# Kernel optimization log

Hardware: AMD Instinct MI355X
Metric: run time of the kernel (lower is better)

Reference implementation:

```python
import jax, jax.numpy as jnp
import numpy as np

G = 8          # num_groups
GIN = 2048 // G   # group_in_features
GOUT = 2048 // G  # group_out_features


def setup_inputs() -> dict:
    key = jax.random.key(0)
    kx, kw, kb = jax.random.split(key, 3)
    x = jax.random.normal(kx, (8192, 2048), dtype=jnp.float32)
    # per-group linear params, torch nn.Linear default init scale ~ U(-1/sqrt(fan_in), ...)
    bound = 1.0 / np.sqrt(GIN)
    W = jax.random.uniform(kw, (G, GIN, GOUT), minval=-bound, maxval=bound, dtype=jnp.float32)
    b = jax.random.uniform(kb, (G, GOUT), minval=-bound, maxval=bound, dtype=jnp.float32)
    # rational activation coeffs, init p=[1,0,0,0], q=[1,0,0] per group
    p = jnp.tile(jnp.array([1.0, 0.0, 0.0, 0.0], dtype=jnp.float32), (G, 1))
    q = jnp.tile(jnp.array([1.0, 0.0, 0.0], dtype=jnp.float32), (G, 1))
    return {"x": x, "W": W, "b": b, "p": p, "q": q}


def _rational(y, p, q):
    # y: [N, G, GOUT]; p: [G, 4]; q: [G, 3] -> broadcast over N and GOUT
    p = p[None, :, :, None]  # [1,G,4,1]
    q = q[None, :, :, None]  # [1,G,3,1]
    y2 = y * y
    y3 = y2 * y
    num = p[:, :, 0] + p[:, :, 1] * y + p[:, :, 2] * y2 + p[:, :, 3] * y3
    den = 1.0 + jnp.abs(q[:, :, 0] * y + q[:, :, 1] * y2 + q[:, :, 2] * y3)
    return num / den


def reference(x, W, b, p, q):
    N = x.shape[0]
    xg = x.reshape(N, G, GIN)                       # chunk along last dim
    y = jnp.einsum('ngi,gio->ngo', xg, W) + b[None]  # grouped GEMM, [N,G,GOUT]
    out = _rational(y, p, q)
    return out.reshape(N, G * GOUT)                 # cat along last dim
```

## Files before the change

### kernel.cpp

```cpp
#include <hip/hip_runtime.h>
#include <hip/hip_bf16.h>

#define G_ 8
#define GIN_ 256
#define GOUT_ 256
#define NROWS_ 8192
#define LDX_ 2048

typedef __attribute__((ext_vector_type(4))) float f32x4;
typedef __attribute__((ext_vector_type(8))) short bf16x8;

__global__ __launch_bounds__(256) void wprep_kernel(const float* __restrict__ W,
                                                    __hip_bfloat16* __restrict__ Wt) {
    __shared__ float tile[64][65];
    const int bid = blockIdx.x;
    const int g  = bid >> 4;
    const int kt = (bid >> 2) & 3;
    const int ct = bid & 3;
    const float* Wg = W + g * (GIN_ * GOUT_);
    __hip_bfloat16* Wo = Wt + (size_t)g * (GIN_ * GOUT_);
    const int lane_o = threadIdx.x & 63;
    const int sub    = threadIdx.x >> 6;
#pragma unroll
    for (int r = 0; r < 16; ++r) {
        int i = r * 4 + sub;
        tile[i][lane_o] = Wg[(kt * 64 + i) * GOUT_ + ct * 64 + lane_o];
    }
    __syncthreads();
    const int col = threadIdx.x & 63;
    const int kgb = threadIdx.x >> 6;
#pragma unroll
    for (int h = 0; h < 2; ++h) {
        const int kg    = kgb + h * 4;
        const int kglob = kt * 64 + kg * 8;
        const int c     = kglob >> 5;
        const int quad  = (kglob >> 3) & 3;
        const int colg  = ct * 64 + col;
        const int cb    = colg >> 4;
        const int c16   = colg & 15;
        union { __hip_bfloat16 hh[8]; bf16x8 v; } cv;
#pragma unroll
        for (int j = 0; j < 8; ++j)
            cv.hh[j] = __float2bfloat16(tile[kg * 8 + j][col]);
        *(bf16x8*)(Wo + (size_t)(c * 16 + cb) * 512 + c16 * 32 + quad * 8) = cv.v;
    }
}

__device__ __forceinline__ bf16x8 cvt8(const f32x4 a, const f32x4 b) {
    union { __hip_bfloat16 h[8]; bf16x8 v; } u;
    u.h[0] = __float2bfloat16(a.x); u.h[1] = __float2bfloat16(a.y);
    u.h[2] = __float2bfloat16(a.z); u.h[3] = __float2bfloat16(a.w);
    u.h[4] = __float2bfloat16(b.x); u.h[5] = __float2bfloat16(b.y);
    u.h[6] = __float2bfloat16(b.z); u.h[7] = __float2bfloat16(b.w);
    return u.v;
}

__global__ __launch_bounds__(512, 4) void gkan_kernel(const float* __restrict__ x,
                                                      const __hip_bfloat16* __restrict__ Wt,
                                                      const float* __restrict__ bias,
                                                      const float* __restrict__ pc,
                                                      const float* __restrict__ qc,
                                                      float* __restrict__ out) {
    __shared__ __align__(16) float As[2][32 * 256];

    const int bid  = blockIdx.x;
    const int g    = bid & 7;
    const int row0 = (bid >> 3) * 128;

    const int t    = threadIdx.x;
    const int wave = t >> 6;
    const int lane = t & 63;
    const int lm   = lane & 15;
    const int q    = lane >> 4;

    const float* xbase = x + (size_t)row0 * LDX_ + g * GIN_;
    const int gsrc = (lane & ~7) | ((lane & 7) ^ wave);

#define DMA_SLAB(s, buf)                                                      \
    {                                                                         \
        const float* xs_ = xbase + (size_t)(s) * 32 * LDX_;                   \
        _Pragma("unroll")                                                     \
        for (int r_ = 0; r_ < 4; ++r_) {                                      \
            const float* src_ = xs_ + (size_t)(r_ * 8 + wave) * LDX_ + gsrc * 4; \
            __builtin_amdgcn_global_load_lds(                                 \
                (const __attribute__((address_space(1))) void*)src_,          \
                (__attribute__((address_space(3))) void*)                     \
                    ((char*)As + (buf) * 32768 + r_ * 8192 + t * 16),         \
                16, 0, 0);                                                    \
        }                                                                     \
    }

    DMA_SLAB(0, 0);

    const __hip_bfloat16* bp = Wt + (size_t)g * (GIN_ * GOUT_)
                                  + (wave * 2) * 512 + lm * 32 + q * 8;
    bf16x8 B0[8], B1[8];
#pragma unroll
    for (int c = 0; c < 8; ++c) {
        B0[c] = *(const bf16x8*)(bp + (size_t)c * (16 * 512));
        B1[c] = *(const bf16x8*)(bp + (size_t)c * (16 * 512) + 512);
    }

    f32x4 bb4[2];
    int col0[2];
#pragma unroll
    for (int nt = 0; nt < 2; ++nt) {
        col0[nt] = g * GOUT_ + wave * 32 + nt * 16 + q * 4;
        bb4[nt]  = *(const f32x4*)(bias + col0[nt]);
    }
    const float p0 = pc[g * 4 + 0], p1 = pc[g * 4 + 1];
    const float p2 = pc[g * 4 + 2], p3 = pc[g * 4 + 3];
    const float q0 = qc[g * 3 + 0], q1 = qc[g * 3 + 1], q2 = qc[g * 3 + 2];

    asm volatile("s_waitcnt vmcnt(0)\n\ts_barrier" ::: "memory");

#pragma unroll 1
    for (int s = 0; s < 4; ++s) {
        const int buf = s & 1;

        if (s < 3) DMA_SLAB(s + 1, buf ^ 1);

        f32x4 acc[2][2] = {};
        const char* ab = (const char*)As + buf * 32768;
#pragma unroll
        for (int c = 0; c < 8; ++c) {
            bf16x8 af[2];
#pragma unroll
            for (int mt = 0; mt < 2; ++mt) {
                const int rr  = mt * 16 + lm;
                const int gg0 = c * 8 + ((q * 2)     ^ (lm & 7));
                const int gg1 = c * 8 + ((q * 2 + 1) ^ (lm & 7));
                const f32x4 lo = *(const f32x4*)(ab + rr * 1024 + gg0 * 16);
                const f32x4 hi = *(const f32x4*)(ab + rr * 1024 + gg1 * 16);
                af[mt] = cvt8(lo, hi);
            }
            acc[0][0] = __builtin_amdgcn_mfma_f32_16x16x32_bf16(B0[c], af[0], acc[0][0], 0, 0, 0);
            acc[0][1] = __builtin_amdgcn_mfma_f32_16x16x32_bf16(B1[c], af[0], acc[0][1], 0, 0, 0);
            acc[1][0] = __builtin_amdgcn_mfma_f32_16x16x32_bf16(B0[c], af[1], acc[1][0], 0, 0, 0);
            acc[1][1] = __builtin_amdgcn_mfma_f32_16x16x32_bf16(B1[c], af[1], acc[1][1], 0, 0, 0);
        }

#pragma unroll
        for (int mt = 0; mt < 2; ++mt) {
            const int row_o = row0 + s * 32 + mt * 16 + lm;
#pragma unroll
            for (int nt = 0; nt < 2; ++nt) {
                f32x4 o;
#pragma unroll
                for (int r = 0; r < 4; ++r) {
                    const float y   = acc[mt][nt][r] + bb4[nt][r];
                    const float num = p0 + y * (p1 + y * (p2 + y * p3));
                    const float den = 1.0f + fabsf(y * (q0 + y * (q1 + y * q2)));
                    o[r] = num * __builtin_amdgcn_rcpf(den);
                }
                *(f32x4*)(out + (size_t)row_o * LDX_ + col0[nt]) = o;
            }
        }

        if (s < 3)
            asm volatile("s_waitcnt vmcnt(4)\n\ts_barrier" ::: "memory");
    }
#undef DMA_SLAB
}

extern "C" void kernel_launch(void* const* d_in, const int* in_sizes, int n_in,
                              void* d_out, int out_size, void* d_ws, size_t ws_size,
                              hipStream_t stream) {
    const float* x = (const float*)d_in[0];
    const float* W = (const float*)d_in[1];
    const float* b = (const float*)d_in[2];
    const float* p = (const float*)d_in[3];
    const float* q = (const float*)d_in[4];
    float* out = (float*)d_out;

    __hip_bfloat16* Wt = (__hip_bfloat16*)d_ws;

    wprep_kernel<<<128, 256, 0, stream>>>(W, Wt);
    gkan_kernel<<<512, 512, 0, stream>>>(x, Wt, b, p, q, out);
}
```

Baseline: 127.3 us.

## Deepen x prefetch pipeline to four 16-row LDS buffers with fully unrolled schedule

```diff
diff --git a/kernel.cpp b/kernel.cpp
--- a/kernel.cpp
+++ b/kernel.cpp
@@ -61,7 +61,7 @@
                                                       const float* __restrict__ pc,
                                                       const float* __restrict__ qc,
                                                       float* __restrict__ out) {
-    __shared__ __align__(16) float As[2][32 * 256];
+    __shared__ __align__(16) float As[4][16 * 256];
 
     const int bid  = blockIdx.x;
     const int g    = bid & 7;
@@ -76,21 +76,52 @@
     const float* xbase = x + (size_t)row0 * LDX_ + g * GIN_;
     const int gsrc = (lane & ~7) | ((lane & 7) ^ wave);
 
-#define DMA_SLAB(s, buf)                                                      \
+#define SB() __builtin_amdgcn_sched_barrier(0)
+#define GATE(N) asm volatile("s_waitcnt vmcnt(" #N ")\n\ts_barrier" ::: "memory")
+
+#define DMA_HS(hs, buf)                                                       \
     {                                                                         \
-        const float* xs_ = xbase + (size_t)(s) * 32 * LDX_;                   \
         _Pragma("unroll")                                                     \
-        for (int r_ = 0; r_ < 4; ++r_) {                                      \
-            const float* src_ = xs_ + (size_t)(r_ * 8 + wave) * LDX_ + gsrc * 4; \
+        for (int r_ = 0; r_ < 2; ++r_) {                                      \
+            const float* src_ = xbase                                         \
+                + (size_t)((hs) * 16 + r_ * 8 + wave) * LDX_ + gsrc * 4;      \
             __builtin_amdgcn_global_load_lds(                                 \
                 (const __attribute__((address_space(1))) void*)src_,          \
                 (__attribute__((address_space(3))) void*)                     \
-                    ((char*)As + (buf) * 32768 + r_ * 8192 + t * 16),         \
+                    ((char*)As + (buf) * 16384 + r_ * 8192 + t * 16),         \
                 16, 0, 0);                                                    \
         }                                                                     \
     }
 
-    DMA_SLAB(0, 0);
+#define DO_HS(hs, buf)                                                        \
+    {                                                                         \
+        f32x4 acc0 = {0.f, 0.f, 0.f, 0.f}, acc1 = {0.f, 0.f, 0.f, 0.f};       \
+        const char* ab_ = (const char*)As + (buf) * 16384 + lm * 1024;        \
+        _Pragma("unroll")                                                     \
+        for (int c_ = 0; c_ < 8; ++c_) {                                      \
+            const int gg0_ = c_ * 8 + ((q * 2)     ^ (lm & 7));               \
+            const int gg1_ = c_ * 8 + ((q * 2 + 1) ^ (lm & 7));               \
+            const f32x4 lo_ = *(const f32x4*)(ab_ + gg0_ * 16);               \
+            const f32x4 hi_ = *(const f32x4*)(ab_ + gg1_ * 16);               \
+            const bf16x8 af_ = cvt8(lo_, hi_);                                \
+            acc0 = __builtin_amdgcn_mfma_f32_16x16x32_bf16(B0[c_], af_, acc0, 0, 0, 0); \
+            acc1 = __builtin_amdgcn_mfma_f32_16x16x32_bf16(B1[c_], af_, acc1, 0, 0, 0); \
+        }                                                                     \
+        const int row_o_ = row0 + (hs) * 16 + lm;                             \
+        _Pragma("unroll")                                                     \
+        for (int nt_ = 0; nt_ < 2; ++nt_) {                                   \
+            const f32x4 a_ = nt_ ? acc1 : acc0;                               \
+            f32x4 o_;                                                         \
+            _Pragma("unroll")                                                 \
+            for (int r_ = 0; r_ < 4; ++r_) {                                  \
+                const float y_   = a_[r_] + bb4[nt_][r_];                     \
+                const float num_ = p0 + y_ * (p1 + y_ * (p2 + y_ * p3));      \
+                const float den_ = 1.0f + fabsf(y_ * (q0 + y_ * (q1 + y_ * q2))); \
+                o_[r_] = num_ * __builtin_amdgcn_rcpf(den_);                  \
+            }                                                                 \
+            *(f32x4*)(out + (size_t)row_o_ * LDX_ + col0[nt_]) = o_;          \
+        }                                                                     \
+    }
 
     const __hip_bfloat16* bp = Wt + (size_t)g * (GIN_ * GOUT_)
                                   + (wave * 2) * 512 + lm * 32 + q * 8;
@@ -100,7 +131,6 @@
         B0[c] = *(const bf16x8*)(bp + (size_t)c * (16 * 512));
         B1[c] = *(const bf16x8*)(bp + (size_t)c * (16 * 512) + 512);
     }
-
     f32x4 bb4[2];
     int col0[2];
 #pragma unroll
@@ -111,56 +141,25 @@
     const float p0 = pc[g * 4 + 0], p1 = pc[g * 4 + 1];
     const float p2 = pc[g * 4 + 2], p3 = pc[g * 4 + 3];
     const float q0 = qc[g * 3 + 0], q1 = qc[g * 3 + 1], q2 = qc[g * 3 + 2];
+    SB();
 
-    asm volatile("s_waitcnt vmcnt(0)\n\ts_barrier" ::: "memory");
+    DMA_HS(0, 0); DMA_HS(1, 1); DMA_HS(2, 2);
+    SB();
+    GATE(4);
 
-#pragma unroll 1
-    for (int s = 0; s < 4; ++s) {
-        const int buf = s & 1;
+    DMA_HS(3, 3); SB(); DO_HS(0, 0); GATE(6);
+    DMA_HS(4, 0); SB(); DO_HS(1, 1); GATE(8);
+    DMA_HS(5, 1); SB(); DO_HS(2, 2); GATE(10);
+    DMA_HS(6, 2); SB(); DO_HS(3, 3); GATE(10);
+    DMA_HS(7, 3); SB(); DO_HS(4, 0); GATE(10);
+    DO_HS(5, 1); GATE(8);
+    DO_HS(6, 2); GATE(6);
+    DO_HS(7, 3);
 
-        if (s < 3) DMA_SLAB(s + 1, buf ^ 1);
-
-        f32x4 acc[2][2] = {};
-        const char* ab = (const char*)As + buf * 32768;
-#pragma unroll
-        for (int c = 0; c < 8; ++c) {
-            bf16x8 af[2];
-#pragma unroll
-            for (int mt = 0; mt < 2; ++mt) {
-                const int rr  = mt * 16 + lm;
-                const int gg0 = c * 8 + ((q * 2)     ^ (lm & 7));
-                const int gg1 = c * 8 + ((q * 2 + 1) ^ (lm & 7));
-                const f32x4 lo = *(const f32x4*)(ab + rr * 1024 + gg0 * 16);
-                const f32x4 hi = *(const f32x4*)(ab + rr * 1024 + gg1 * 16);
-                af[mt] = cvt8(lo, hi);
-            }
-            acc[0][0] = __builtin_amdgcn_mfma_f32_16x16x32_bf16(B0[c], af[0], acc[0][0], 0, 0, 0);
-            acc[0][1] = __builtin_amdgcn_mfma_f32_16x16x32_bf16(B1[c], af[0], acc[0][1], 0, 0, 0);
-            acc[1][0] = __builtin_amdgcn_mfma_f32_16x16x32_bf16(B0[c], af[1], acc[1][0], 0, 0, 0);
-            acc[1][1] = __builtin_amdgcn_mfma_f32_16x16x32_bf16(B1[c], af[1], acc[1][1], 0, 0, 0);
-        }
-
-#pragma unroll
-        for (int mt = 0; mt < 2; ++mt) {
-            const int row_o = row0 + s * 32 + mt * 16 + lm;
-#pragma unroll
-            for (int nt = 0; nt < 2; ++nt) {
-                f32x4 o;
-#pragma unroll
-                for (int r = 0; r < 4; ++r) {
-                    const float y   = acc[mt][nt][r] + bb4[nt][r];
-                    const float num = p0 + y * (p1 + y * (p2 + y * p3));
-                    const float den = 1.0f + fabsf(y * (q0 + y * (q1 + y * q2)));
-                    o[r] = num * __builtin_amdgcn_rcpf(den);
-                }
-                *(f32x4*)(out + (size_t)row_o * LDX_ + col0[nt]) = o;
-            }
-        }
-
-        if (s < 3)
-            asm volatile("s_waitcnt vmcnt(4)\n\ts_barrier" ::: "memory");
-    }
-#undef DMA_SLAB
+#undef DMA_HS
+#undef DO_HS
+#undef GATE
+#undef SB
 }
 
 extern "C" void kernel_launch(void* const* d_in, const int* in_sizes, int n_in,
```

New measurement: 126.8 us (median of 2 runs). About the same (-0.4%).
